# Kernel optimization log

Hardware: AMD Instinct MI355X
Metric: run time of the kernel (lower is better)

Reference implementation:

```python
import jax, jax.numpy as jnp
import numpy as np

NUM_EXPERTS = 8
TOP_K = 2
HIDDEN = 2048
INTER = 2048
SWIGLU_LIMIT = 7.0
BATCH, SEQ = 4, 2048


def setup_inputs() -> dict:
    key = jax.random.key(0)
    k0, k1, k2, k3, k4 = jax.random.split(key, 5)
    x = jax.random.normal(k0, (BATCH, SEQ, HIDDEN), jnp.float32)
    Wr = jax.random.normal(k1, (HIDDEN, NUM_EXPERTS), jnp.float32) * 0.02
    Wg = jax.random.normal(k2, (NUM_EXPERTS, HIDDEN, INTER), jnp.float32) * 0.02
    Wu = jax.random.normal(k3, (NUM_EXPERTS, HIDDEN, INTER), jnp.float32) * 0.02
    Wd = jax.random.normal(k4, (NUM_EXPERTS, INTER, HIDDEN), jnp.float32) * 0.02
    return {"hidden_states": x, "Wr": Wr, "Wg": Wg, "Wu": Wu, "Wd": Wd}


def reference(hidden_states, Wr, Wg, Wu, Wd):
    # Router: logits [B,S,E], top-k over experts, softmax over the k logits.
    router_logits = jnp.einsum('bsh,he->bse', hidden_states, Wr)
    topk_logits, selected = jax.lax.top_k(router_logits, TOP_K)  # [B,S,K]
    router_probs = jax.nn.softmax(topk_logits, axis=-1)          # [B,S,K]

    # Per-expert masked-dense SwiGLU. Because the Dense layers have no bias,
    # Expert(x * mask) == Expert(x) at selected positions and the combine
    # weight is 0 elsewhere, so running on unmasked x is mathematically
    # identical to the original's masked-input formulation.
    out = jnp.zeros_like(hidden_states)
    for e in range(NUM_EXPERTS):  # fixed structural loop over experts
        w_e = jnp.where(selected == e, router_probs, 0.0).sum(axis=-1, keepdims=True)  # [B,S,1]
        g = jnp.einsum('bsh,hi->bsi', hidden_states, Wg[e])
        g = jnp.clip(jax.nn.silu(g), -SWIGLU_LIMIT, SWIGLU_LIMIT)
        u = jnp.einsum('bsh,hi->bsi', hidden_states, Wu[e])
        h = jnp.einsum('bsi,ih->bsh', g * u, Wd[e])
        out = out + h * w_e
    return out
```

## Files before the change

### kernel.cpp

```cpp
#include <hip/hip_runtime.h>

#define TOKENS 8192
#define HID 2048
#define NEXP 8
#define NT 32

typedef float f32x4 __attribute__((ext_vector_type(4)));
typedef short bf16x8 __attribute__((ext_vector_type(8)));

#define WS_XBF     0ULL
#define WS_ACT     33554432ULL
#define WS_WCAT    100663296ULL
#define WS_WDT     234881024ULL
#define WS_ROWTOK  301989888ULL
#define WS_ROWPROB 302055424ULL
#define WS_EIDX    302120960ULL
#define WS_PROBS   302186496ULL
#define WS_META    302252032ULL

__device__ __forceinline__ unsigned short f2bf(float f) {
    union { float f; unsigned int u; } a; a.f = f;
    unsigned int r = a.u + 0x7fffu + ((a.u >> 16) & 1u);
    return (unsigned short)(r >> 16);
}

__device__ __forceinline__ void gload16(void* ldsdst, const void* gsrc) {
    __builtin_amdgcn_global_load_lds(
        (const __attribute__((address_space(1))) void*)gsrc,
        (__attribute__((address_space(3))) void*)ldsdst, 16, 0, 0);
}

#define BAR asm volatile("s_barrier" ::: "memory")
#define VM4 asm volatile("s_waitcnt vmcnt(4)" ::: "memory")
#define VM0 asm volatile("s_waitcnt vmcnt(0)" ::: "memory")

__global__ __launch_bounds__(256) void router_kernel(
    const float* __restrict__ x, const float* __restrict__ Wr,
    unsigned short* __restrict__ xbf, int2* __restrict__ eidx,
    float2* __restrict__ probs, int* __restrict__ meta) {
    __shared__ float wrt[NEXP * HID];
    int tid = threadIdx.x;
    for (int f = tid; f < HID * NEXP; f += 256) {
        int i = f >> 3, e = f & 7;
        wrt[e * HID + i] = Wr[f];
    }
    __syncthreads();
    int w = tid >> 6, l = tid & 63;
    int tok = blockIdx.x * 4 + w;
    const float4* xr = (const float4*)(x + (size_t)tok * HID);
    float acc[NEXP];
#pragma unroll
    for (int e = 0; e < NEXP; ++e) acc[e] = 0.f;
    unsigned long long* xbr = (unsigned long long*)(xbf + (size_t)tok * HID);
#pragma unroll
    for (int it = 0; it < 8; ++it) {
        float4 v = xr[it * 64 + l];
        int k0 = (it * 64 + l) * 4;
#pragma unroll
        for (int e = 0; e < NEXP; ++e) {
            float4 wv = *(const float4*)&wrt[e * HID + k0];
            acc[e] += v.x * wv.x + v.y * wv.y + v.z * wv.z + v.w * wv.w;
        }
        unsigned long long pk = (unsigned long long)f2bf(v.x)
                              | ((unsigned long long)f2bf(v.y) << 16)
                              | ((unsigned long long)f2bf(v.z) << 32)
                              | ((unsigned long long)f2bf(v.w) << 48);
        int qi = ((k0 >> 5) << 3) + (((k0 >> 2) & 3) << 1) + ((k0 >> 4) & 1);
        xbr[qi] = pk;
    }
#pragma unroll
    for (int e = 0; e < NEXP; ++e) {
#pragma unroll
        for (int d = 1; d < 64; d <<= 1) acc[e] += __shfl_xor(acc[e], d, 64);
    }
    if (l == 0) {
        int e0 = 0; float v0 = acc[0];
#pragma unroll
        for (int e = 1; e < NEXP; ++e) if (acc[e] > v0) { v0 = acc[e]; e0 = e; }
        int e1 = -1; float v1 = 0.f;
#pragma unroll
        for (int e = 0; e < NEXP; ++e)
            if (e != e0 && (e1 < 0 || acc[e] > v1)) { v1 = acc[e]; e1 = e; }
        float a = __expf(v1 - v0);
        float inv = 1.f / (1.f + a);
        int2 ei; ei.x = e0; ei.y = e1;
        float2 pp; pp.x = inv; pp.y = a * inv;
        eidx[tok] = ei;
        probs[tok] = pp;
        atomicAdd(&meta[e0], 1);
        atomicAdd(&meta[e1], 1);
    }
}

__global__ __launch_bounds__(256) void convert_kernel(
    const float* __restrict__ Wg, const float* __restrict__ Wu,
    const float* __restrict__ Wd, unsigned short* __restrict__ wcat,
    unsigned short* __restrict__ wdt) {
    int mz = blockIdx.z;
    int mat = mz >> 3, e = mz & 7;
    const float* W = (mat == 0 ? Wg : (mat == 1 ? Wu : Wd)) + (size_t)e * HID * HID;
    int kb = blockIdx.y * 64, nb = blockIdx.x * 64;
    __shared__ unsigned short t[64][68];
    int tid = threadIdx.x;
    int kr = tid >> 4;
    int nc = (tid & 15) * 4;
#pragma unroll
    for (int ki = 0; ki < 4; ++ki) {
        int k = kr + ki * 16;
        float4 v = *(const float4*)&W[(size_t)(kb + k) * HID + nb + nc];
        t[nc + 0][k] = f2bf(v.x);
        t[nc + 1][k] = f2bf(v.y);
        t[nc + 2][k] = f2bf(v.z);
        t[nc + 3][k] = f2bf(v.w);
    }
    __syncthreads();
    int q = tid & 15;
    int k0 = ((q >> 3) << 5) + (((q >> 1) & 3) << 2) + ((q & 1) << 4);
#pragma unroll
    for (int ni = 0; ni < 4; ++ni) {
        int n = (tid >> 4) + ni * 16;
        int gn = nb + n;
        unsigned short* orow;
        if (mat < 2)
            orow = wcat + ((size_t)e * 4096 + (gn >> 4) * 32 + mat * 16 + (gn & 15)) * HID;
        else
            orow = wdt + ((size_t)e * HID + gn) * HID;
        unsigned long long pk = (unsigned long long)t[n][k0]
                              | ((unsigned long long)t[n][k0 + 1] << 16)
                              | ((unsigned long long)t[n][k0 + 2] << 32)
                              | ((unsigned long long)t[n][k0 + 3] << 48);
        *(unsigned long long*)&orow[kb + q * 4] = pk;
    }
}

__global__ void scan_kernel(int* __restrict__ meta) {
    if (threadIdx.x == 0) {
        int s = 0;
#pragma unroll
        for (int e = 0; e < NEXP; ++e) { meta[16 + e] = s; s += meta[e]; }
    }
}

__global__ __launch_bounds__(256) void build_kernel(
    const int2* __restrict__ eidx, const float2* __restrict__ probs,
    int* __restrict__ meta, int* __restrict__ row_token, float* __restrict__ row_prob) {
    int t = blockIdx.x * 256 + threadIdx.x;
    if (t >= TOKENS) return;
    int2 e = eidx[t];
    float2 p = probs[t];
    int s0 = meta[16 + e.x] + atomicAdd(&meta[8 + e.x], 1);
    row_token[s0] = t; row_prob[s0] = p.x;
    int s1 = meta[16 + e.y] + atomicAdd(&meta[8 + e.y], 1);
    row_token[s1] = t; row_prob[s1] = p.y;
}

#define STA(dn, kh, tt) { char* _d = lds + (dn)*32768 + (kh)*16384 + tid*16; \
    gload16(_d,        a0 + (tt)*64 + (kh)*32); \
    gload16(_d + 8192, a1 + (tt)*64 + (kh)*32); }
#define STB(dn, kh, tt) { char* _d = lds + (dn)*32768 + 65536 + (kh)*16384 + tid*16; \
    gload16(_d,        b0 + (tt)*64 + (kh)*32); \
    gload16(_d + 8192, b1 + (tt)*64 + (kh)*32); }
#define LDA(d, kh) { const char* _b = lds + (d)*32768 + (kh)*16384 + afo; \
    af[0] = *(const bf16x8*)(_b);          af[1] = *(const bf16x8*)(_b + 1024); \
    af[2] = *(const bf16x8*)(_b + 2048);   af[3] = *(const bf16x8*)(_b + 3072); \
    af[4] = *(const bf16x8*)(_b + 4096);   af[5] = *(const bf16x8*)(_b + 5120); \
    af[6] = *(const bf16x8*)(_b + 6144);   af[7] = *(const bf16x8*)(_b + 7168); }
#define LDB(d, kh, nn) (*(const bf16x8*)(lds + (d)*32768 + (kh)*16384 + bfo + (nn)*1024))
#define MM(n0, n1) do { \
    __builtin_amdgcn_s_setprio(1); \
    _Pragma("unroll") \
    for (int m = 0; m < 8; ++m) { \
        acc[m][n0] = __builtin_amdgcn_mfma_f32_16x16x32_bf16(af[m], bq0, acc[m][n0], 0, 0, 0); \
        acc[m][n1] = __builtin_amdgcn_mfma_f32_16x16x32_bf16(af[m], bq1, acc[m][n1], 0, 0, 0); \
    } \
    __builtin_amdgcn_s_setprio(0); \
} while (0)

#define GEMM_MAIN_LOOP \
    { STA(0, 0, 0); STB(0, 0, 0); STA(0, 1, 0); STB(0, 1, 0); } \
    VM4; BAR; \
    for (int t = 0; t < NT - 1; ++t) { \
        const int d = t & 1, dn = d ^ 1, tn = t + 1; \
        bf16x8 bq0, bq1; \
        LDA(d, 0); bq0 = LDB(d, 0, 0); bq1 = LDB(d, 0, 1); \
        STA(dn, 0, tn); \
        MM(0, 1); \
        BAR; \
        bq0 = LDB(d, 0, 2); bq1 = LDB(d, 0, 3); \
        STB(dn, 0, tn); \
        MM(2, 3); \
        VM4; BAR; \
        LDA(d, 1); bq0 = LDB(d, 1, 0); bq1 = LDB(d, 1, 1); \
        STA(dn, 1, tn); \
        MM(0, 1); \
        BAR; \
        bq0 = LDB(d, 1, 2); bq1 = LDB(d, 1, 3); \
        STB(dn, 1, tn); \
        MM(2, 3); \
        VM4; BAR; \
    } \
    { const int d = (NT - 1) & 1; \
        bf16x8 bq0, bq1; \
        LDA(d, 0); bq0 = LDB(d, 0, 0); bq1 = LDB(d, 0, 1); MM(0, 1); \
        bq0 = LDB(d, 0, 2); bq1 = LDB(d, 0, 3); MM(2, 3); \
        VM0; BAR; \
        LDA(d, 1); bq0 = LDB(d, 1, 0); bq1 = LDB(d, 1, 1); MM(0, 1); \
        bq0 = LDB(d, 1, 2); bq1 = LDB(d, 1, 3); MM(2, 3); \
    }

__global__ __launch_bounds__(512) void gemm1_kernel(
    const unsigned short* __restrict__ xbf, const unsigned short* __restrict__ wcat,
    const int* __restrict__ row_token, const int* __restrict__ meta,
    unsigned short* __restrict__ act) {
    int e = blockIdx.z;
    int cnt = meta[e];
    int rt = blockIdx.y;
    if (rt * 256 >= cnt) return;
    int off = meta[16 + e];
    int ct = blockIdx.x;
    __shared__ __align__(16) char lds[131072];
    int tid = threadIdx.x, w = tid >> 6, l = tid & 63;
    int wr = w >> 2, wc = w & 3;
    int r16 = l & 15, g = l >> 4;

    int srow = tid >> 2;
    int sxu = (tid & 3) ^ ((tid >> 3) & 3);
    int rr0 = rt * 256 + srow;       if (rr0 >= cnt) rr0 = cnt - 1;
    int rr1 = rt * 256 + srow + 128; if (rr1 >= cnt) rr1 = cnt - 1;
    const unsigned short* a0 = xbf + (size_t)row_token[off + rr0] * HID + sxu * 8;
    const unsigned short* a1 = xbf + (size_t)row_token[off + rr1] * HID + sxu * 8;
    const unsigned short* b0 = wcat + ((size_t)(e * 4096 + ct * 256 + srow)) * HID + sxu * 8;
    const unsigned short* b1 = b0 + (size_t)128 * HID;

    int sw = (r16 >> 1) & 3;
    int afo = (wr * 128 + r16) * 64 + (g ^ sw) * 16;
    int bfo = 65536 + (wc * 64 + r16) * 64 + (g ^ sw) * 16;

    f32x4 acc[8][4];
    f32x4 z = {0.f, 0.f, 0.f, 0.f};
#pragma unroll
    for (int m = 0; m < 8; ++m)
#pragma unroll
        for (int nn = 0; nn < 4; ++nn) acc[m][nn] = z;
    bf16x8 af[8];

    GEMM_MAIN_LOOP

    int pb = (ct * 4 + wc) * 32 + (r16 >> 2) * 8 + (r16 & 3);
#pragma unroll
    for (int m = 0; m < 8; ++m) {
        int rbase = wr * 128 + m * 16 + (l >> 4) * 4;
#pragma unroll
        for (int q = 0; q < 4; ++q) {
            int r = rt * 256 + rbase + q;
            if (r < cnt) {
                unsigned short* arow = act + (size_t)(off + r) * HID;
#pragma unroll
                for (int p = 0; p < 2; ++p) {
                    float gg = acc[m][2 * p][q];
                    float uu = acc[m][2 * p + 1][q];
                    float s = gg / (1.f + __expf(-gg));
                    s = fminf(fmaxf(s, -7.f), 7.f);
                    arow[pb + p * 4] = f2bf(s * uu);
                }
            }
        }
    }
}

__global__ __launch_bounds__(512) void gemm2_kernel(
    const unsigned short* __restrict__ act, const unsigned short* __restrict__ wdt,
    const int* __restrict__ row_token, const float* __restrict__ row_prob,
    const int* __restrict__ meta, float* __restrict__ out) {
    int e = blockIdx.z;
    int cnt = meta[e];
    int rt = blockIdx.y;
    if (rt * 256 >= cnt) return;
    int off = meta[16 + e];
    int ct = blockIdx.x;
    __shared__ __align__(16) char lds[131072];
    int tid = threadIdx.x, w = tid >> 6, l = tid & 63;
    int wr = w >> 2, wc = w & 3;
    int r16 = l & 15, g = l >> 4;

    int srow = tid >> 2;
    int sxu = (tid & 3) ^ ((tid >> 3) & 3);
    int rr0 = rt * 256 + srow;       if (rr0 >= cnt) rr0 = cnt - 1;
    int rr1 = rt * 256 + srow + 128; if (rr1 >= cnt) rr1 = cnt - 1;
    const unsigned short* a0 = act + (size_t)(off + rr0) * HID + sxu * 8;
    const unsigned short* a1 = act + (size_t)(off + rr1) * HID + sxu * 8;
    const unsigned short* b0 = wdt + ((size_t)(e * HID + ct * 256 + srow)) * HID + sxu * 8;
    const unsigned short* b1 = b0 + (size_t)128 * HID;

    int sw = (r16 >> 1) & 3;
    int afo = (wr * 128 + r16) * 64 + (g ^ sw) * 16;
    int bfo = 65536 + (wc * 64 + r16) * 64 + (g ^ sw) * 16;

    f32x4 acc[8][4];
    f32x4 z = {0.f, 0.f, 0.f, 0.f};
#pragma unroll
    for (int m = 0; m < 8; ++m)
#pragma unroll
        for (int nn = 0; nn < 4; ++nn) acc[m][nn] = z;
    bf16x8 af[8];

    GEMM_MAIN_LOOP

    int colb = ct * 256 + wc * 64;
#pragma unroll
    for (int m = 0; m < 8; ++m) {
        int rbase = wr * 128 + m * 16 + (l >> 4) * 4;
#pragma unroll
        for (int q = 0; q < 4; ++q) {
            int r = rt * 256 + rbase + q;
            if (r < cnt) {
                int slot = off + r;
                int tok = row_token[slot];
                float pr = row_prob[slot];
                float* orow = out + (size_t)tok * HID + colb;
#pragma unroll
                for (int nn = 0; nn < 4; ++nn)
                    unsafeAtomicAdd(&orow[nn * 16 + r16], acc[m][nn][q] * pr);
            }
        }
    }
}

extern "C" void kernel_launch(void* const* d_in, const int* in_sizes, int n_in,
                              void* d_out, int out_size, void* d_ws, size_t ws_size,
                              hipStream_t stream) {
    const float* x  = (const float*)d_in[0];
    const float* Wr = (const float*)d_in[1];
    const float* Wg = (const float*)d_in[2];
    const float* Wu = (const float*)d_in[3];
    const float* Wd = (const float*)d_in[4];
    float* out = (float*)d_out;
    char* ws = (char*)d_ws;

    unsigned short* xbf  = (unsigned short*)(ws + WS_XBF);
    unsigned short* act  = (unsigned short*)(ws + WS_ACT);
    unsigned short* wcat = (unsigned short*)(ws + WS_WCAT);
    unsigned short* wdt  = (unsigned short*)(ws + WS_WDT);
    int* row_token  = (int*)(ws + WS_ROWTOK);
    float* row_prob = (float*)(ws + WS_ROWPROB);
    int2* eidx      = (int2*)(ws + WS_EIDX);
    float2* probs   = (float2*)(ws + WS_PROBS);
    int* meta       = (int*)(ws + WS_META);

    hipMemsetAsync(d_out, 0, (size_t)out_size * sizeof(float), stream);
    hipMemsetAsync(meta, 0, 64, stream);

    hipLaunchKernelGGL(convert_kernel, dim3(32, 32, 24), dim3(256), 0, stream,
                       Wg, Wu, Wd, wcat, wdt);
    hipLaunchKernelGGL(router_kernel, dim3(TOKENS / 4), dim3(256), 0, stream,
                       x, Wr, xbf, eidx, probs, meta);
    hipLaunchKernelGGL(scan_kernel, dim3(1), dim3(64), 0, stream, meta);
    hipLaunchKernelGGL(build_kernel, dim3(TOKENS / 256), dim3(256), 0, stream,
                       eidx, probs, meta, row_token, row_prob);
    hipLaunchKernelGGL(gemm1_kernel, dim3(16, 64, NEXP), dim3(512), 0, stream,
                       xbf, wcat, row_token, meta, act);
    hipLaunchKernelGGL(gemm2_kernel, dim3(8, 64, NEXP), dim3(512), 0, stream,
                       act, wdt, row_token, row_prob, meta, out);
}
```

Before: 908.7 us.

## Double-buffer A fragments and prefetch LDS reads ahead of MFMA blocks

```diff
diff --git a/kernel.cpp b/kernel.cpp
--- a/kernel.cpp
+++ b/kernel.cpp
@@ -160,52 +160,53 @@
 #define STB(dn, kh, tt) { char* _d = lds + (dn)*32768 + 65536 + (kh)*16384 + tid*16; \
     gload16(_d,        b0 + (tt)*64 + (kh)*32); \
     gload16(_d + 8192, b1 + (tt)*64 + (kh)*32); }
-#define LDA(d, kh) { const char* _b = lds + (d)*32768 + (kh)*16384 + afo; \
-    af[0] = *(const bf16x8*)(_b);          af[1] = *(const bf16x8*)(_b + 1024); \
-    af[2] = *(const bf16x8*)(_b + 2048);   af[3] = *(const bf16x8*)(_b + 3072); \
-    af[4] = *(const bf16x8*)(_b + 4096);   af[5] = *(const bf16x8*)(_b + 5120); \
-    af[6] = *(const bf16x8*)(_b + 6144);   af[7] = *(const bf16x8*)(_b + 7168); }
+#define LDA_TO(dst, d, kh) { const char* _b = lds + (d)*32768 + (kh)*16384 + afo; \
+    dst[0] = *(const bf16x8*)(_b);        dst[1] = *(const bf16x8*)(_b + 1024); \
+    dst[2] = *(const bf16x8*)(_b + 2048); dst[3] = *(const bf16x8*)(_b + 3072); \
+    dst[4] = *(const bf16x8*)(_b + 4096); dst[5] = *(const bf16x8*)(_b + 5120); \
+    dst[6] = *(const bf16x8*)(_b + 6144); dst[7] = *(const bf16x8*)(_b + 7168); }
 #define LDB(d, kh, nn) (*(const bf16x8*)(lds + (d)*32768 + (kh)*16384 + bfo + (nn)*1024))
-#define MM(n0, n1) do { \
+#define MM(A, B0, B1, n0, n1) do { \
     __builtin_amdgcn_s_setprio(1); \
     _Pragma("unroll") \
     for (int m = 0; m < 8; ++m) { \
-        acc[m][n0] = __builtin_amdgcn_mfma_f32_16x16x32_bf16(af[m], bq0, acc[m][n0], 0, 0, 0); \
-        acc[m][n1] = __builtin_amdgcn_mfma_f32_16x16x32_bf16(af[m], bq1, acc[m][n1], 0, 0, 0); \
+        acc[m][n0] = __builtin_amdgcn_mfma_f32_16x16x32_bf16(A[m], B0, acc[m][n0], 0, 0, 0); \
+        acc[m][n1] = __builtin_amdgcn_mfma_f32_16x16x32_bf16(A[m], B1, acc[m][n1], 0, 0, 0); \
     } \
     __builtin_amdgcn_s_setprio(0); \
 } while (0)
 
 #define GEMM_MAIN_LOOP \
-    { STA(0, 0, 0); STB(0, 0, 0); STA(0, 1, 0); STB(0, 1, 0); } \
+    bf16x8 af[8], af2[8], bq0, bq1, bq2, bq3; \
+    STA(0, 0, 0); STB(0, 0, 0); STA(0, 1, 0); STB(0, 1, 0); \
     VM4; BAR; \
+    LDA_TO(af, 0, 0); bq0 = LDB(0, 0, 0); bq1 = LDB(0, 0, 1); \
     for (int t = 0; t < NT - 1; ++t) { \
         const int d = t & 1, dn = d ^ 1, tn = t + 1; \
-        bf16x8 bq0, bq1; \
-        LDA(d, 0); bq0 = LDB(d, 0, 0); bq1 = LDB(d, 0, 1); \
+        bq2 = LDB(d, 0, 2); bq3 = LDB(d, 0, 3); \
         STA(dn, 0, tn); \
-        MM(0, 1); \
-        BAR; \
-        bq0 = LDB(d, 0, 2); bq1 = LDB(d, 0, 3); \
+        MM(af, bq0, bq1, 0, 1); \
         STB(dn, 0, tn); \
-        MM(2, 3); \
         VM4; BAR; \
-        LDA(d, 1); bq0 = LDB(d, 1, 0); bq1 = LDB(d, 1, 1); \
+        LDA_TO(af2, d, 1); bq0 = LDB(d, 1, 0); bq1 = LDB(d, 1, 1); \
+        MM(af, bq2, bq3, 2, 3); \
+        bq2 = LDB(d, 1, 2); bq3 = LDB(d, 1, 3); \
         STA(dn, 1, tn); \
-        MM(0, 1); \
-        BAR; \
-        bq0 = LDB(d, 1, 2); bq1 = LDB(d, 1, 3); \
+        MM(af2, bq0, bq1, 0, 1); \
         STB(dn, 1, tn); \
-        MM(2, 3); \
         VM4; BAR; \
+        LDA_TO(af, dn, 0); bq0 = LDB(dn, 0, 0); bq1 = LDB(dn, 0, 1); \
+        MM(af2, bq2, bq3, 2, 3); \
     } \
     { const int d = (NT - 1) & 1; \
-        bf16x8 bq0, bq1; \
-        LDA(d, 0); bq0 = LDB(d, 0, 0); bq1 = LDB(d, 0, 1); MM(0, 1); \
-        bq0 = LDB(d, 0, 2); bq1 = LDB(d, 0, 3); MM(2, 3); \
+        bq2 = LDB(d, 0, 2); bq3 = LDB(d, 0, 3); \
+        MM(af, bq0, bq1, 0, 1); \
         VM0; BAR; \
-        LDA(d, 1); bq0 = LDB(d, 1, 0); bq1 = LDB(d, 1, 1); MM(0, 1); \
-        bq0 = LDB(d, 1, 2); bq1 = LDB(d, 1, 3); MM(2, 3); \
+        LDA_TO(af2, d, 1); bq0 = LDB(d, 1, 0); bq1 = LDB(d, 1, 1); \
+        MM(af, bq2, bq3, 2, 3); \
+        bq2 = LDB(d, 1, 2); bq3 = LDB(d, 1, 3); \
+        MM(af2, bq0, bq1, 0, 1); \
+        MM(af2, bq2, bq3, 2, 3); \
     }
 
 __global__ __launch_bounds__(512) void gemm1_kernel(
@@ -242,7 +243,6 @@
     for (int m = 0; m < 8; ++m)
 #pragma unroll
         for (int nn = 0; nn < 4; ++nn) acc[m][nn] = z;
-    bf16x8 af[8];
 
     GEMM_MAIN_LOOP
 
@@ -302,7 +302,6 @@
     for (int m = 0; m < 8; ++m)
 #pragma unroll
         for (int nn = 0; nn < 4; ++nn) acc[m][nn] = z;
-    bf16x8 af[8];
 
     GEMM_MAIN_LOOP
 
```

Result: no change. 910.8 us (+0.2%).
